# Optimization experiments

Hardware: AMD Instinct MI355X
Metric: run time of the kernel (lower is better)

## Reference

```python
import jax, jax.numpy as jnp
import numpy as np

MASK_OD = np.array([
    [False, False, False, True, True, True, True, False, False],
    [False, False, True, True, True, True, True, True, False],
    [False, True, True, True, True, True, True, True, True],
    [True, True, True, True, True, True, True, False, True],
    [True, True, True, True, True, True, True, False, True],
    [False, True, True, True, True, True, True, True, True],
    [False, False, True, True, True, True, True, True, False],
    [False, False, False, True, True, True, True, False, False]], dtype=bool)

SCALE = float(np.sqrt(128.0))  # sqrt(attn_dim)


def build_prior(num_points=52):
    # Faithful reproduction of _init_anatomical_prior (OD laterality, no flip)
    pr_grid = np.arange(196) // 14
    pc_grid = np.arange(196) % 14
    prior = np.zeros((num_points, 196), dtype=np.float32)
    vf_idx = 0
    for r in range(8):
        for c in range(9):
            if MASK_OD[r, c]:
                pr = 13 - int(r * 13 / 7)
                pc = 13 - int(c * 13 / 8)
                prior[vf_idx] = -((pr_grid - pr) ** 2 + (pc_grid - pc) ** 2) / (2.0 * 3.0 ** 2)
                vf_idx += 1
    return prior


def setup_inputs() -> dict:
    key = jax.random.key(0)
    ks = jax.random.split(key, 8)
    B, P, K, E, A = 256, 52, 196, 1024, 128
    return {
        "patches": jax.random.normal(ks[0], (B, K, E), jnp.float32),
        "queries": jax.random.normal(ks[1], (P, A), jnp.float32) * 0.02,
        "Wk": jax.random.normal(ks[2], (A, E), jnp.float32) / np.sqrt(E),
        "Wv": jax.random.normal(ks[3], (A, E), jnp.float32) / np.sqrt(E),
        "Wo": jax.random.normal(ks[4], (E, A), jnp.float32) / np.sqrt(A),
        "bo": jnp.zeros((E,), jnp.float32),
        "patch_pos": jax.random.normal(ks[5], (K, A), jnp.float32) * 0.02,
        "temperature": jnp.asarray(2.0, jnp.float32),
        "attn_prior": jnp.asarray(build_prior(P)),
    }


def reference(patches, queries, Wk, Wv, Wo, bo, patch_pos, temperature, attn_prior):
    # patches: [B, 196, E]; laterality fixed to 'OD' (no prior flip)
    keys = jnp.einsum('bke,ae->bka', patches, Wk) + patch_pos  # [B, 196, A]
    vals = jnp.einsum('bke,ae->bka', patches, Wv)              # [B, 196, A]
    logits = jnp.einsum('qa,bka->bqk', queries, keys) / SCALE  # [B, 52, 196]
    temp = jax.nn.softplus(temperature) + 0.5
    logits = (logits + attn_prior[None]) / temp
    attn_weights = jax.nn.softmax(logits, axis=-1)
    # dropout is identity in eval mode
    attended = jnp.einsum('bqk,bka->bqa', attn_weights, vals)  # [B, 52, A]
    out = jnp.einsum('bqa,ea->bqe', attended, Wo) + bo         # [B, 52, E]
    return out, attn_weights
```

## Files before the change

### kernel.cpp

```cpp
#include <hip/hip_runtime.h>

typedef __attribute__((ext_vector_type(8))) short bf16x8;
typedef __attribute__((ext_vector_type(4))) short bf16x4;
typedef __attribute__((ext_vector_type(4))) float f32x4;
typedef __attribute__((ext_vector_type(4))) float floatx4;

__device__ __forceinline__ unsigned short f2bf(float f) {
    unsigned int u = __float_as_uint(f);
    u += 0x7fffu + ((u >> 16) & 1u);
    return (unsigned short)(u >> 16);
}
__device__ __forceinline__ float bf2f_s(short h) {
    return __uint_as_float(((unsigned int)(unsigned short)h) << 16);
}

__device__ __forceinline__ bf16x8 cvt8(f32x4 lo, f32x4 hi) {
    union { unsigned int u[4]; bf16x8 v; } r;
    asm("v_cvt_pk_bf16_f32 %0, %1, %2" : "=v"(r.u[0]) : "v"(lo[0]), "v"(lo[1]));
    asm("v_cvt_pk_bf16_f32 %0, %1, %2" : "=v"(r.u[1]) : "v"(lo[2]), "v"(lo[3]));
    asm("v_cvt_pk_bf16_f32 %0, %1, %2" : "=v"(r.u[2]) : "v"(hi[0]), "v"(hi[1]));
    asm("v_cvt_pk_bf16_f32 %0, %1, %2" : "=v"(r.u[3]) : "v"(hi[2]), "v"(hi[3]));
    return r.v;
}
__device__ __forceinline__ bf16x4 cvt4(f32x4 v) {
    union { unsigned int u[2]; bf16x4 x; } r;
    asm("v_cvt_pk_bf16_f32 %0, %1, %2" : "=v"(r.u[0]) : "v"(v[0]), "v"(v[1]));
    asm("v_cvt_pk_bf16_f32 %0, %1, %2" : "=v"(r.u[1]) : "v"(v[2]), "v"(v[3]));
    return r.x;
}

__global__ void k_convert(const float* __restrict__ Wk, const float* __restrict__ Wv,
                          const float* __restrict__ Wo,
                          unsigned short* __restrict__ Wkvb, unsigned short* __restrict__ Wob) {
    int i = (blockIdx.x * blockDim.x + threadIdx.x) * 4;
    if (i < 131072) {
        floatx4 a = *reinterpret_cast<const floatx4*>(Wk + i);
        floatx4 b = *reinterpret_cast<const floatx4*>(Wv + i);
        floatx4 c = *reinterpret_cast<const floatx4*>(Wo + i);
        *reinterpret_cast<bf16x4*>(Wkvb + i)          = cvt4(a);
        *reinterpret_cast<bf16x4*>(Wkvb + 131072 + i) = cvt4(b);
        *reinterpret_cast<bf16x4*>(Wob + i)           = cvt4(c);
    }
}

__global__ __launch_bounds__(512)
void k_keysvals(const float* __restrict__ patches,
                const unsigned short* __restrict__ Wkvb,
                const float* __restrict__ patch_pos,
                unsigned short* __restrict__ kv)
{
    __shared__ unsigned short As[2][208][72];
    __shared__ unsigned short Bs[2][256][72];

    const int tid  = threadIdx.x;
    const int lane = tid & 63;
    const int w    = tid >> 6;
    const int l15  = lane & 15;
    const int lg   = lane >> 4;
    const int b    = blockIdx.x;
    const float* abase = patches + (size_t)b * 196 * 1024;

    const int brow = tid >> 1;
    const int bh   = tid & 1;
    const unsigned short* bgp = Wkvb + (size_t)brow * 1024 + bh * 32;

    f32x4  aH[7];
    bf16x8 bH[4];

    f32x4 acc[13][2];
    #pragma unroll
    for (int i = 0; i < 13; ++i) {
        acc[i][0] = (f32x4){0.f, 0.f, 0.f, 0.f};
        acc[i][1] = (f32x4){0.f, 0.f, 0.f, 0.f};
    }

    auto issue = [&](int t) {
        const int ko = t * 64;
        #pragma unroll
        for (int i = 0; i < 6; ++i) {
            int g = tid + i * 512;
            int r = g >> 4, gc = g & 15;
            aH[i] = *reinterpret_cast<const f32x4*>(abase + (size_t)r * 1024 + ko + gc * 4);
        }
        if (tid < 64) {
            int g = 3072 + tid;
            int r = g >> 4, gc = g & 15;
            aH[6] = *reinterpret_cast<const f32x4*>(abase + (size_t)r * 1024 + ko + gc * 4);
        }
        #pragma unroll
        for (int j = 0; j < 4; ++j)
            bH[j] = *reinterpret_cast<const bf16x8*>(bgp + ko + j * 8);
    };
    auto store = [&](int buf) {
        #pragma unroll
        for (int i = 0; i < 6; ++i) {
            int g = tid + i * 512;
            int r = g >> 4, gc = g & 15;
            *reinterpret_cast<bf16x4*>(&As[buf][r][gc * 4]) = cvt4(aH[i]);
        }
        if (tid < 64) {
            int g = 3072 + tid;
            int r = g >> 4, gc = g & 15;
            *reinterpret_cast<bf16x4*>(&As[buf][r][gc * 4]) = cvt4(aH[6]);
        }
        #pragma unroll
        for (int j = 0; j < 4; ++j)
            *reinterpret_cast<bf16x8*>(&Bs[buf][brow][bh * 32 + j * 8]) = bH[j];
    };
    auto compute = [&](int buf) {
        #pragma unroll
        for (int kk = 0; kk < 2; ++kk) {
            bf16x8 bf[2];
            #pragma unroll
            for (int nf = 0; nf < 2; ++nf)
                bf[nf] = *reinterpret_cast<const bf16x8*>(&Bs[buf][w * 32 + nf * 16 + l15][kk * 32 + lg * 8]);
            #pragma unroll
            for (int mf = 0; mf < 13; ++mf) {
                bf16x8 af = *reinterpret_cast<const bf16x8*>(&As[buf][mf * 16 + l15][kk * 32 + lg * 8]);
                acc[mf][0] = __builtin_amdgcn_mfma_f32_16x16x32_bf16(af, bf[0], acc[mf][0], 0, 0, 0);
                acc[mf][1] = __builtin_amdgcn_mfma_f32_16x16x32_bf16(af, bf[1], acc[mf][1], 0, 0, 0);
            }
        }
    };

    issue(0);
    store(0);
    __syncthreads();

    for (int t = 0; t < 16; ++t) {
        if (t < 15) issue(t + 1);
        compute(t & 1);
        if (t < 15) store((t + 1) & 1);
        __syncthreads();
    }

    #pragma unroll
    for (int mf = 0; mf < 13; ++mf) {
        #pragma unroll
        for (int i = 0; i < 4; ++i) {
            int ml = mf * 16 + lg * 4 + i;
            if (ml < 196) {
                #pragma unroll
                for (int nf = 0; nf < 2; ++nf) {
                    int n = w * 32 + nf * 16 + l15;
                    float v = acc[mf][nf][i];
                    if (n < 128) v += patch_pos[ml * 128 + n];
                    kv[((size_t)b * 196 + ml) * 256 + n] = f2bf(v);
                }
            }
        }
    }
}

__global__ __launch_bounds__(1024)
void k_attn(const unsigned short* __restrict__ kv,
            const float* __restrict__ queries,
            const float* __restrict__ prior,
            const float* __restrict__ temperature,
            float* __restrict__ attn_out,
            unsigned short* __restrict__ att)
{
    __shared__ unsigned short k_s[196][136];
    __shared__ unsigned short v_s[196][128];
    __shared__ unsigned short q_s[52][128];
    __shared__ float          l_s[52][196];

    const int b   = blockIdx.x;
    const int tid = threadIdx.x;
    const size_t base = (size_t)b * 196 * 256;

    for (int idx = tid; idx < 6272; idx += 1024) {
        int row = idx >> 5;
        int c   = (idx & 31) * 8;
        bf16x8 v = *reinterpret_cast<const bf16x8*>(kv + base + row * 256 + c);
        if (c < 128) *reinterpret_cast<bf16x8*>(&k_s[row][c])       = v;
        else         *reinterpret_cast<bf16x8*>(&v_s[row][c - 128]) = v;
    }
    for (int idx = tid; idx < 1664; idx += 1024) {
        int row = idx >> 5;
        int c   = (idx & 31) * 4;
        const float* qp = queries + row * 128 + c;
        bf16x4 sv;
        sv[0] = (short)f2bf(qp[0]); sv[1] = (short)f2bf(qp[1]);
        sv[2] = (short)f2bf(qp[2]); sv[3] = (short)f2bf(qp[3]);
        *reinterpret_cast<bf16x4*>(&q_s[row][c]) = sv;
    }
    __syncthreads();

    const float inv_temp  = 1.0f / (log1pf(expf(temperature[0])) + 0.5f);
    const float inv_scale = 0.08838834764831845f;

    for (int task = tid; task < 3328; task += 1024) {
        int q  = task >> 6;
        int kg = task & 63;
        if (kg < 49) {
            float dot0 = 0.f, dot1 = 0.f, dot2 = 0.f, dot3 = 0.f;
            #pragma unroll 4
            for (int c = 0; c < 128; c += 8) {
                bf16x8 qv = *reinterpret_cast<const bf16x8*>(&q_s[q][c]);
                float qf[8];
                #pragma unroll
                for (int e = 0; e < 8; ++e) qf[e] = bf2f_s(qv[e]);
                bf16x8 k0v = *reinterpret_cast<const bf16x8*>(&k_s[kg][c]);
                bf16x8 k1v = *reinterpret_cast<const bf16x8*>(&k_s[kg + 49][c]);
                bf16x8 k2v = *reinterpret_cast<const bf16x8*>(&k_s[kg + 98][c]);
                bf16x8 k3v = *reinterpret_cast<const bf16x8*>(&k_s[kg + 147][c]);
                #pragma unroll
                for (int e = 0; e < 8; ++e) {
                    dot0 += qf[e] * bf2f_s(k0v[e]);
                    dot1 += qf[e] * bf2f_s(k1v[e]);
                    dot2 += qf[e] * bf2f_s(k2v[e]);
                    dot3 += qf[e] * bf2f_s(k3v[e]);
                }
            }
            int k;
            k = kg;       l_s[q][k] = (dot0 * inv_scale + prior[q * 196 + k]) * inv_temp;
            k = kg + 49;  l_s[q][k] = (dot1 * inv_scale + prior[q * 196 + k]) * inv_temp;
            k = kg + 98;  l_s[q][k] = (dot2 * inv_scale + prior[q * 196 + k]) * inv_temp;
            k = kg + 147; l_s[q][k] = (dot3 * inv_scale + prior[q * 196 + k]) * inv_temp;
        }
    }
    __syncthreads();

    const int lane = tid & 63;
    const int wave = tid >> 6;
    for (int q = wave; q < 52; q += 16) {
        float x0 = l_s[q][lane];
        float x1 = l_s[q][lane + 64];
        float x2 = l_s[q][lane + 128];
        float x3 = (lane < 4) ? l_s[q][lane + 192] : -1e30f;
        float m = fmaxf(fmaxf(x0, x1), fmaxf(x2, x3));
        #pragma unroll
        for (int off = 32; off > 0; off >>= 1) m = fmaxf(m, __shfl_xor(m, off));
        float e0 = expf(x0 - m), e1 = expf(x1 - m), e2 = expf(x2 - m);
        float e3 = (lane < 4) ? expf(x3 - m) : 0.0f;
        float s = e0 + e1 + e2 + e3;
        #pragma unroll
        for (int off = 32; off > 0; off >>= 1) s += __shfl_xor(s, off);
        float inv = 1.0f / s;
        float* po = attn_out + ((size_t)b * 52 + q) * 196;
        float a0 = e0 * inv, a1 = e1 * inv, a2 = e2 * inv;
        l_s[q][lane]       = a0;  po[lane]       = a0;
        l_s[q][lane + 64]  = a1;  po[lane + 64]  = a1;
        l_s[q][lane + 128] = a2;  po[lane + 128] = a2;
        if (lane < 4) { float a3 = e3 * inv; l_s[q][lane + 192] = a3; po[lane + 192] = a3; }
    }
    __syncthreads();

    if (tid < 832) {
        int q  = tid >> 4;
        int a0 = (tid & 15) * 8;
        float accv[8] = {0.f, 0.f, 0.f, 0.f, 0.f, 0.f, 0.f, 0.f};
        for (int k = 0; k < 196; ++k) {
            float wgt = l_s[q][k];
            bf16x8 vv = *reinterpret_cast<const bf16x8*>(&v_s[k][a0]);
            #pragma unroll
            for (int e = 0; e < 8; ++e) accv[e] += wgt * bf2f_s(vv[e]);
        }
        bf16x8 sv;
        #pragma unroll
        for (int e = 0; e < 8; ++e) sv[e] = (short)f2bf(accv[e]);
        *reinterpret_cast<bf16x8*>(att + ((size_t)b * 52 + q) * 128 + a0) = sv;
    }
}

__global__ __launch_bounds__(512)
void k_out(const unsigned short* __restrict__ att,
           const unsigned short* __restrict__ Wob,
           const float* __restrict__ bo,
           float* __restrict__ out)
{
    __shared__ unsigned short As[64][72];
    __shared__ unsigned short Bs[256][72];

    const int tid  = threadIdx.x;
    const int lane = tid & 63;
    const int wave = tid >> 6;
    const int wm   = wave >> 2;
    const int wn   = wave & 3;
    const int l15  = lane & 15;
    const int lg   = lane >> 4;
    const int row0 = blockIdx.x * 64;
    const int e0   = blockIdx.y * 256;

    f32x4 acc[2][4];
    #pragma unroll
    for (int i = 0; i < 2; ++i)
        #pragma unroll
        for (int j = 0; j < 4; ++j)
            acc[i][j] = (f32x4){0.f, 0.f, 0.f, 0.f};

    for (int ko = 0; ko < 128; ko += 64) {
        {
            int r = tid >> 3;
            int c = (tid & 7) * 8;
            bf16x8 v = *reinterpret_cast<const bf16x8*>(att + (size_t)(row0 + r) * 128 + ko + c);
            *reinterpret_cast<bf16x8*>(&As[r][c]) = v;
        }
        {
            int r = tid >> 3;
            int c = (tid & 7) * 8;
            #pragma unroll
            for (int it = 0; it < 4; ++it) {
                bf16x8 v = *reinterpret_cast<const bf16x8*>(Wob + (size_t)(e0 + it * 64 + r) * 128 + ko + c);
                *reinterpret_cast<bf16x8*>(&Bs[it * 64 + r][c]) = v;
            }
        }
        __syncthreads();
        #pragma unroll
        for (int kk = 0; kk < 2; ++kk) {
            bf16x8 af[2], bfr[4];
            #pragma unroll
            for (int mi = 0; mi < 2; ++mi)
                af[mi] = *reinterpret_cast<const bf16x8*>(&As[wm * 32 + mi * 16 + l15][kk * 32 + lg * 8]);
            #pragma unroll
            for (int ni = 0; ni < 4; ++ni)
                bfr[ni] = *reinterpret_cast<const bf16x8*>(&Bs[wn * 64 + ni * 16 + l15][kk * 32 + lg * 8]);
            #pragma unroll
            for (int mi = 0; mi < 2; ++mi)
                #pragma unroll
                for (int ni = 0; ni < 4; ++ni)
                    acc[mi][ni] = __builtin_amdgcn_mfma_f32_16x16x32_bf16(af[mi], bfr[ni], acc[mi][ni], 0, 0, 0);
        }
        __syncthreads();
    }
    #pragma unroll
    for (int mi = 0; mi < 2; ++mi) {
        #pragma unroll
        for (int i = 0; i < 4; ++i) {
            int m = row0 + wm * 32 + mi * 16 + lg * 4 + i;
            #pragma unroll
            for (int ni = 0; ni < 4; ++ni) {
                int e = e0 + wn * 64 + ni * 16 + l15;
                out[(size_t)m * 1024 + e] = acc[mi][ni][i] + bo[e];
            }
        }
    }
}

extern "C" void kernel_launch(void* const* d_in, const int* in_sizes, int n_in,
                              void* d_out, int out_size, void* d_ws, size_t ws_size,
                              hipStream_t stream)
{
    const float* patches     = (const float*)d_in[0];
    const float* queries     = (const float*)d_in[1];
    const float* Wk          = (const float*)d_in[2];
    const float* Wv          = (const float*)d_in[3];
    const float* Wo          = (const float*)d_in[4];
    const float* bo          = (const float*)d_in[5];
    const float* patch_pos   = (const float*)d_in[6];
    const float* temperature = (const float*)d_in[7];
    const float* prior       = (const float*)d_in[8];

    float* out      = (float*)d_out;
    float* attn_out = out + (size_t)256 * 52 * 1024;

    unsigned short* Wkvb = (unsigned short*)d_ws;
    unsigned short* Wob  = Wkvb + 256 * 1024;
    unsigned short* kv   = Wob + 1024 * 128;
    unsigned short* att  = kv + (size_t)50176 * 256;

    k_convert <<<128, 256, 0, stream>>>(Wk, Wv, Wo, Wkvb, Wob);
    k_keysvals<<<256, 512, 0, stream>>>(patches, Wkvb, patch_pos, kv);
    k_attn    <<<256, 1024, 0, stream>>>(kv, queries, prior, temperature, attn_out, att);
    k_out     <<<dim3(208, 4), 512, 0, stream>>>(att, Wob, bo, out);
}
```

Before: 145.8 us.

## Fuse key/value projection with attention kernel, keep K/V in shared memory

Merges the K/V projection GEMM and the attention kernel into one 512-thread kernel per batch. K and V are written to shared memory instead of a global bf16 buffer, removing a global round trip and one launch. The GEMM main loop now uses two register prefetch sets with explicit waitcnt barriers to deepen the pipeline. In exchange the attention phase runs with half the threads per block, and the large shared memory footprint limits occupancy to one block per CU.

Result: slower. 170.7 us (+17.1%).

```diff
diff --git a/kernel.cpp b/kernel.cpp
--- a/kernel.cpp
+++ b/kernel.cpp
@@ -12,15 +12,6 @@
 }
 __device__ __forceinline__ float bf2f_s(short h) {
     return __uint_as_float(((unsigned int)(unsigned short)h) << 16);
-}
-
-__device__ __forceinline__ bf16x8 cvt8(f32x4 lo, f32x4 hi) {
-    union { unsigned int u[4]; bf16x8 v; } r;
-    asm("v_cvt_pk_bf16_f32 %0, %1, %2" : "=v"(r.u[0]) : "v"(lo[0]), "v"(lo[1]));
-    asm("v_cvt_pk_bf16_f32 %0, %1, %2" : "=v"(r.u[1]) : "v"(lo[2]), "v"(lo[3]));
-    asm("v_cvt_pk_bf16_f32 %0, %1, %2" : "=v"(r.u[2]) : "v"(hi[0]), "v"(hi[1]));
-    asm("v_cvt_pk_bf16_f32 %0, %1, %2" : "=v"(r.u[3]) : "v"(hi[2]), "v"(hi[3]));
-    return r.v;
 }
 __device__ __forceinline__ bf16x4 cvt4(f32x4 v) {
     union { unsigned int u[2]; bf16x4 x; } r;
@@ -44,13 +35,16 @@
 }
 
 __global__ __launch_bounds__(512)
-void k_keysvals(const float* __restrict__ patches,
-                const unsigned short* __restrict__ Wkvb,
-                const float* __restrict__ patch_pos,
-                unsigned short* __restrict__ kv)
+void k_fused(const float* __restrict__ patches,
+             const unsigned short* __restrict__ Wkvb,
+             const float* __restrict__ patch_pos,
+             const float* __restrict__ queries,
+             const float* __restrict__ prior,
+             const float* __restrict__ temperature,
+             float* __restrict__ attn_out,
+             unsigned short* __restrict__ att)
 {
-    __shared__ unsigned short As[2][208][72];
-    __shared__ unsigned short Bs[2][256][72];
+    __shared__ char smem[157568];
 
     const int tid  = threadIdx.x;
     const int lane = tid & 63;
@@ -64,9 +58,6 @@
     const int bh   = tid & 1;
     const unsigned short* bgp = Wkvb + (size_t)brow * 1024 + bh * 32;
 
-    f32x4  aH[7];
-    bf16x8 bH[4];
-
     f32x4 acc[13][2];
     #pragma unroll
     for (int i = 0; i < 13; ++i) {
@@ -74,65 +65,84 @@
         acc[i][1] = (f32x4){0.f, 0.f, 0.f, 0.f};
     }
 
-    auto issue = [&](int t) {
-        const int ko = t * 64;
-        #pragma unroll
-        for (int i = 0; i < 6; ++i) {
-            int g = tid + i * 512;
-            int r = g >> 4, gc = g & 15;
-            aH[i] = *reinterpret_cast<const f32x4*>(abase + (size_t)r * 1024 + ko + gc * 4);
-        }
-        if (tid < 64) {
-            int g = 3072 + tid;
-            int r = g >> 4, gc = g & 15;
-            aH[6] = *reinterpret_cast<const f32x4*>(abase + (size_t)r * 1024 + ko + gc * 4);
-        }
-        #pragma unroll
-        for (int j = 0; j < 4; ++j)
-            bH[j] = *reinterpret_cast<const bf16x8*>(bgp + ko + j * 8);
-    };
-    auto store = [&](int buf) {
-        #pragma unroll
-        for (int i = 0; i < 6; ++i) {
-            int g = tid + i * 512;
-            int r = g >> 4, gc = g & 15;
-            *reinterpret_cast<bf16x4*>(&As[buf][r][gc * 4]) = cvt4(aH[i]);
-        }
-        if (tid < 64) {
-            int g = 3072 + tid;
-            int r = g >> 4, gc = g & 15;
-            *reinterpret_cast<bf16x4*>(&As[buf][r][gc * 4]) = cvt4(aH[6]);
-        }
-        #pragma unroll
-        for (int j = 0; j < 4; ++j)
-            *reinterpret_cast<bf16x8*>(&Bs[buf][brow][bh * 32 + j * 8]) = bH[j];
-    };
-    auto compute = [&](int buf) {
-        #pragma unroll
-        for (int kk = 0; kk < 2; ++kk) {
-            bf16x8 bf[2];
-            #pragma unroll
-            for (int nf = 0; nf < 2; ++nf)
-                bf[nf] = *reinterpret_cast<const bf16x8*>(&Bs[buf][w * 32 + nf * 16 + l15][kk * 32 + lg * 8]);
-            #pragma unroll
-            for (int mf = 0; mf < 13; ++mf) {
-                bf16x8 af = *reinterpret_cast<const bf16x8*>(&As[buf][mf * 16 + l15][kk * 32 + lg * 8]);
-                acc[mf][0] = __builtin_amdgcn_mfma_f32_16x16x32_bf16(af, bf[0], acc[mf][0], 0, 0, 0);
-                acc[mf][1] = __builtin_amdgcn_mfma_f32_16x16x32_bf16(af, bf[1], acc[mf][1], 0, 0, 0);
-            }
-        }
-    };
-
-    issue(0);
-    store(0);
-    __syncthreads();
-
-    for (int t = 0; t < 16; ++t) {
-        if (t < 15) issue(t + 1);
-        compute(t & 1);
-        if (t < 15) store((t + 1) & 1);
-        __syncthreads();
-    }
+    f32x4  a0H[7], a1H[7];
+    bf16x8 b0H[4], b1H[4];
+
+#define ISSUE(AH, BH, T)                                                          \
+    do { const int ko_ = (T) * 64;                                                \
+        _Pragma("unroll")                                                         \
+        for (int i_ = 0; i_ < 6; ++i_) {                                          \
+            int g_ = tid + i_ * 512; int r_ = g_ >> 4, gc_ = g_ & 15;             \
+            AH[i_] = *reinterpret_cast<const f32x4*>(abase + (size_t)r_ * 1024 + ko_ + gc_ * 4); \
+        }                                                                         \
+        if (tid < 64) { int g_ = 3072 + tid; int r_ = g_ >> 4, gc_ = g_ & 15;     \
+            AH[6] = *reinterpret_cast<const f32x4*>(abase + (size_t)r_ * 1024 + ko_ + gc_ * 4); } \
+        _Pragma("unroll")                                                         \
+        for (int j_ = 0; j_ < 4; ++j_)                                            \
+            BH[j_] = *reinterpret_cast<const bf16x8*>(bgp + ko_ + j_ * 8);        \
+    } while (0)
+
+#define STORE(AH, BH, BUF)                                                        \
+    do { unsigned short* As_ = (unsigned short*)(smem + (BUF) * 29952);           \
+         unsigned short* Bs_ = (unsigned short*)(smem + 59904 + (BUF) * 36864);   \
+        _Pragma("unroll")                                                         \
+        for (int i_ = 0; i_ < 6; ++i_) {                                          \
+            int g_ = tid + i_ * 512; int r_ = g_ >> 4, gc_ = g_ & 15;             \
+            *reinterpret_cast<bf16x4*>(As_ + r_ * 72 + gc_ * 4) = cvt4(AH[i_]);   \
+        }                                                                         \
+        if (tid < 64) { int g_ = 3072 + tid; int r_ = g_ >> 4, gc_ = g_ & 15;     \
+            *reinterpret_cast<bf16x4*>(As_ + r_ * 72 + gc_ * 4) = cvt4(AH[6]); }  \
+        _Pragma("unroll")                                                         \
+        for (int j_ = 0; j_ < 4; ++j_)                                            \
+            *reinterpret_cast<bf16x8*>(Bs_ + brow * 72 + bh * 32 + j_ * 8) = BH[j_]; \
+    } while (0)
+
+#define COMPUTE(BUF)                                                              \
+    do { const unsigned short* As_ = (const unsigned short*)(smem + (BUF) * 29952); \
+         const unsigned short* Bs_ = (const unsigned short*)(smem + 59904 + (BUF) * 36864); \
+        _Pragma("unroll")                                                         \
+        for (int kk_ = 0; kk_ < 2; ++kk_) {                                       \
+            bf16x8 bf0 = *reinterpret_cast<const bf16x8*>(Bs_ + (w * 32 + l15) * 72 + kk_ * 32 + lg * 8);      \
+            bf16x8 bf1 = *reinterpret_cast<const bf16x8*>(Bs_ + (w * 32 + 16 + l15) * 72 + kk_ * 32 + lg * 8); \
+            _Pragma("unroll")                                                     \
+            for (int mf_ = 0; mf_ < 13; ++mf_) {                                  \
+                bf16x8 af = *reinterpret_cast<const bf16x8*>(As_ + (mf_ * 16 + l15) * 72 + kk_ * 32 + lg * 8); \
+                acc[mf_][0] = __builtin_amdgcn_mfma_f32_16x16x32_bf16(af, bf0, acc[mf_][0], 0, 0, 0); \
+                acc[mf_][1] = __builtin_amdgcn_mfma_f32_16x16x32_bf16(af, bf1, acc[mf_][1], 0, 0, 0); \
+            }                                                                     \
+        }                                                                         \
+    } while (0)
+
+#define FENCE                                                                     \
+    do { __builtin_amdgcn_sched_barrier(0);                                       \
+         asm volatile("s_waitcnt lgkmcnt(0)" ::: "memory");                       \
+         __builtin_amdgcn_s_barrier();                                            \
+         __builtin_amdgcn_sched_barrier(0); } while (0)
+
+    ISSUE(a0H, b0H, 0);
+    STORE(a0H, b0H, 0);
+    ISSUE(a1H, b1H, 1);
+    FENCE;
+
+    for (int tb = 0; tb < 16; tb += 2) {
+        if (tb + 2 < 16) ISSUE(a0H, b0H, tb + 2);
+        COMPUTE(0);
+        STORE(a1H, b1H, 1);
+        FENCE;
+        if (tb + 3 < 16) ISSUE(a1H, b1H, tb + 3);
+        COMPUTE(1);
+        if (tb + 1 < 15) STORE(a0H, b0H, 0);
+        FENCE;
+    }
+#undef ISSUE
+#undef STORE
+#undef COMPUTE
+#undef FENCE
+
+    unsigned short (*k_s)[136] = (unsigned short (*)[136])(smem);
+    unsigned short (*v_s)[128] = (unsigned short (*)[128])(smem + 53312);
+    unsigned short (*q_s)[128] = (unsigned short (*)[128])(smem + 103488);
+    float          (*l_s)[196] = (float (*)[196])(smem + 116800);
 
     #pragma unroll
     for (int mf = 0; mf < 13; ++mf) {
@@ -144,53 +154,24 @@
                 for (int nf = 0; nf < 2; ++nf) {
                     int n = w * 32 + nf * 16 + l15;
                     float v = acc[mf][nf][i];
-                    if (n < 128) v += patch_pos[ml * 128 + n];
-                    kv[((size_t)b * 196 + ml) * 256 + n] = f2bf(v);
+                    if (n < 128) k_s[ml][n] = f2bf(v + patch_pos[ml * 128 + n]);
+                    else         v_s[ml][n - 128] = f2bf(v);
                 }
             }
         }
     }
-}
-
-__global__ __launch_bounds__(1024)
-void k_attn(const unsigned short* __restrict__ kv,
-            const float* __restrict__ queries,
-            const float* __restrict__ prior,
-            const float* __restrict__ temperature,
-            float* __restrict__ attn_out,
-            unsigned short* __restrict__ att)
-{
-    __shared__ unsigned short k_s[196][136];
-    __shared__ unsigned short v_s[196][128];
-    __shared__ unsigned short q_s[52][128];
-    __shared__ float          l_s[52][196];
-
-    const int b   = blockIdx.x;
-    const int tid = threadIdx.x;
-    const size_t base = (size_t)b * 196 * 256;
-
-    for (int idx = tid; idx < 6272; idx += 1024) {
-        int row = idx >> 5;
-        int c   = (idx & 31) * 8;
-        bf16x8 v = *reinterpret_cast<const bf16x8*>(kv + base + row * 256 + c);
-        if (c < 128) *reinterpret_cast<bf16x8*>(&k_s[row][c])       = v;
-        else         *reinterpret_cast<bf16x8*>(&v_s[row][c - 128]) = v;
-    }
-    for (int idx = tid; idx < 1664; idx += 1024) {
+    for (int idx = tid; idx < 1664; idx += 512) {
         int row = idx >> 5;
         int c   = (idx & 31) * 4;
-        const float* qp = queries + row * 128 + c;
-        bf16x4 sv;
-        sv[0] = (short)f2bf(qp[0]); sv[1] = (short)f2bf(qp[1]);
-        sv[2] = (short)f2bf(qp[2]); sv[3] = (short)f2bf(qp[3]);
-        *reinterpret_cast<bf16x4*>(&q_s[row][c]) = sv;
+        f32x4 qv = *reinterpret_cast<const f32x4*>(queries + row * 128 + c);
+        *reinterpret_cast<bf16x4*>(&q_s[row][c]) = cvt4(qv);
     }
     __syncthreads();
 
     const float inv_temp  = 1.0f / (log1pf(expf(temperature[0])) + 0.5f);
     const float inv_scale = 0.08838834764831845f;
 
-    for (int task = tid; task < 3328; task += 1024) {
+    for (int task = tid; task < 3328; task += 512) {
         int q  = task >> 6;
         int kg = task & 63;
         if (kg < 49) {
@@ -222,9 +203,7 @@
     }
     __syncthreads();
 
-    const int lane = tid & 63;
-    const int wave = tid >> 6;
-    for (int q = wave; q < 52; q += 16) {
+    for (int q = w; q < 52; q += 8) {
         float x0 = l_s[q][lane];
         float x1 = l_s[q][lane + 64];
         float x2 = l_s[q][lane + 128];
@@ -247,9 +226,9 @@
     }
     __syncthreads();
 
-    if (tid < 832) {
-        int q  = tid >> 4;
-        int a0 = (tid & 15) * 8;
+    for (int task = tid; task < 832; task += 512) {
+        int q  = task >> 4;
+        int a0 = (task & 15) * 8;
         float accv[8] = {0.f, 0.f, 0.f, 0.f, 0.f, 0.f, 0.f, 0.f};
         for (int k = 0; k < 196; ++k) {
             float wgt = l_s[q][k];
@@ -356,12 +335,11 @@
     float* attn_out = out + (size_t)256 * 52 * 1024;
 
     unsigned short* Wkvb = (unsigned short*)d_ws;
-    unsigned short* Wob  = Wkvb + 256 * 1024;
-    unsigned short* kv   = Wob + 1024 * 128;
-    unsigned short* att  = kv + (size_t)50176 * 256;
-
-    k_convert <<<128, 256, 0, stream>>>(Wk, Wv, Wo, Wkvb, Wob);
-    k_keysvals<<<256, 512, 0, stream>>>(patches, Wkvb, patch_pos, kv);
-    k_attn    <<<256, 1024, 0, stream>>>(kv, queries, prior, temperature, attn_out, att);
-    k_out     <<<dim3(208, 4), 512, 0, stream>>>(att, Wob, bo, out);
-}
+    unsigned short* Wob  = Wkvb + 262144;
+    unsigned short* att  = Wob + 131072;
+
+    k_convert<<<128, 256, 0, stream>>>(Wk, Wv, Wo, Wkvb, Wob);
+    k_fused  <<<256, 512, 0, stream>>>(patches, Wkvb, patch_pos, queries, prior,
+                                       temperature, attn_out, att);
+    k_out    <<<dim3(208, 4), 512, 0, stream>>>(att, Wob, bo, out);
+}
```

## Restructure K/V projection GEMM to 1024 threads with K=32 double-buffered pipeline

Applied to the files above, without the earlier changes.

The K/V projection kernel now runs 1024 threads per block, with each wave owning a 16-column slice instead of 32. The K step per stage drops from 64 to 32, and the loop is rewritten with explicit register ping-pong buffers, sched_barrier fences and a raw s_barrier. The goal is more waves per CU to hide the latency of the fp32 patch loads and less register pressure from accumulators, at the cost of twice as many barriers and a smaller MFMA batch between syncs. The query load in the attention kernel is also vectorized.

After: 137.1 us (median of 2 runs). 1.06x faster.

```diff
diff --git a/kernel.cpp b/kernel.cpp
--- a/kernel.cpp
+++ b/kernel.cpp
@@ -12,15 +12,6 @@
 }
 __device__ __forceinline__ float bf2f_s(short h) {
     return __uint_as_float(((unsigned int)(unsigned short)h) << 16);
-}
-
-__device__ __forceinline__ bf16x8 cvt8(f32x4 lo, f32x4 hi) {
-    union { unsigned int u[4]; bf16x8 v; } r;
-    asm("v_cvt_pk_bf16_f32 %0, %1, %2" : "=v"(r.u[0]) : "v"(lo[0]), "v"(lo[1]));
-    asm("v_cvt_pk_bf16_f32 %0, %1, %2" : "=v"(r.u[1]) : "v"(lo[2]), "v"(lo[3]));
-    asm("v_cvt_pk_bf16_f32 %0, %1, %2" : "=v"(r.u[2]) : "v"(hi[0]), "v"(hi[1]));
-    asm("v_cvt_pk_bf16_f32 %0, %1, %2" : "=v"(r.u[3]) : "v"(hi[2]), "v"(hi[3]));
-    return r.v;
 }
 __device__ __forceinline__ bf16x4 cvt4(f32x4 v) {
     union { unsigned int u[2]; bf16x4 x; } r;
@@ -43,14 +34,13 @@
     }
 }
 
-__global__ __launch_bounds__(512)
+__global__ __launch_bounds__(1024, 4)
 void k_keysvals(const float* __restrict__ patches,
                 const unsigned short* __restrict__ Wkvb,
                 const float* __restrict__ patch_pos,
                 unsigned short* __restrict__ kv)
 {
-    __shared__ unsigned short As[2][208][72];
-    __shared__ unsigned short Bs[2][256][72];
+    __shared__ char smem[74240];
 
     const int tid  = threadIdx.x;
     const int lane = tid & 63;
@@ -60,79 +50,71 @@
     const int b    = blockIdx.x;
     const float* abase = patches + (size_t)b * 196 * 1024;
 
-    const int brow = tid >> 1;
-    const int bh   = tid & 1;
-    const unsigned short* bgp = Wkvb + (size_t)brow * 1024 + bh * 32;
-
-    f32x4  aH[7];
-    bf16x8 bH[4];
-
-    f32x4 acc[13][2];
+    const int ar0 = tid >> 3,          ac0 = tid & 7;
+    const int ar1 = (1024 + tid) >> 3, ac1 = (1024 + tid) & 7;
+    const int br = tid >> 2, bc = tid & 3;
+    const unsigned short* bgp = Wkvb + (size_t)br * 1024 + bc * 8;
+
+    f32x4  a0A, a0B, a1A, a1B;
+    bf16x8 b0H, b1H;
+
+    f32x4 acc[13];
     #pragma unroll
-    for (int i = 0; i < 13; ++i) {
-        acc[i][0] = (f32x4){0.f, 0.f, 0.f, 0.f};
-        acc[i][1] = (f32x4){0.f, 0.f, 0.f, 0.f};
-    }
-
-    auto issue = [&](int t) {
-        const int ko = t * 64;
-        #pragma unroll
-        for (int i = 0; i < 6; ++i) {
-            int g = tid + i * 512;
-            int r = g >> 4, gc = g & 15;
-            aH[i] = *reinterpret_cast<const f32x4*>(abase + (size_t)r * 1024 + ko + gc * 4);
-        }
-        if (tid < 64) {
-            int g = 3072 + tid;
-            int r = g >> 4, gc = g & 15;
-            aH[6] = *reinterpret_cast<const f32x4*>(abase + (size_t)r * 1024 + ko + gc * 4);
-        }
-        #pragma unroll
-        for (int j = 0; j < 4; ++j)
-            bH[j] = *reinterpret_cast<const bf16x8*>(bgp + ko + j * 8);
-    };
-    auto store = [&](int buf) {
-        #pragma unroll
-        for (int i = 0; i < 6; ++i) {
-            int g = tid + i * 512;
-            int r = g >> 4, gc = g & 15;
-            *reinterpret_cast<bf16x4*>(&As[buf][r][gc * 4]) = cvt4(aH[i]);
-        }
-        if (tid < 64) {
-            int g = 3072 + tid;
-            int r = g >> 4, gc = g & 15;
-            *reinterpret_cast<bf16x4*>(&As[buf][r][gc * 4]) = cvt4(aH[6]);
-        }
-        #pragma unroll
-        for (int j = 0; j < 4; ++j)
-            *reinterpret_cast<bf16x8*>(&Bs[buf][brow][bh * 32 + j * 8]) = bH[j];
-    };
-    auto compute = [&](int buf) {
-        #pragma unroll
-        for (int kk = 0; kk < 2; ++kk) {
-            bf16x8 bf[2];
-            #pragma unroll
-            for (int nf = 0; nf < 2; ++nf)
-                bf[nf] = *reinterpret_cast<const bf16x8*>(&Bs[buf][w * 32 + nf * 16 + l15][kk * 32 + lg * 8]);
-            #pragma unroll
-            for (int mf = 0; mf < 13; ++mf) {
-                bf16x8 af = *reinterpret_cast<const bf16x8*>(&As[buf][mf * 16 + l15][kk * 32 + lg * 8]);
-                acc[mf][0] = __builtin_amdgcn_mfma_f32_16x16x32_bf16(af, bf[0], acc[mf][0], 0, 0, 0);
-                acc[mf][1] = __builtin_amdgcn_mfma_f32_16x16x32_bf16(af, bf[1], acc[mf][1], 0, 0, 0);
-            }
-        }
-    };
-
-    issue(0);
-    store(0);
-    __syncthreads();
-
-    for (int t = 0; t < 16; ++t) {
-        if (t < 15) issue(t + 1);
-        compute(t & 1);
-        if (t < 15) store((t + 1) & 1);
-        __syncthreads();
-    }
+    for (int i = 0; i < 13; ++i) acc[i] = (f32x4){0.f, 0.f, 0.f, 0.f};
+
+#define ISSUE(AA, AB, BH, T)                                                       \
+    do { const int ko_ = (T) * 32;                                                 \
+        AA = *reinterpret_cast<const f32x4*>(abase + (size_t)ar0 * 1024 + ko_ + ac0 * 4); \
+        if (tid < 544)                                                             \
+            AB = *reinterpret_cast<const f32x4*>(abase + (size_t)ar1 * 1024 + ko_ + ac1 * 4); \
+        BH = *reinterpret_cast<const bf16x8*>(bgp + (T) * 32);                     \
+    } while (0)
+
+#define STORE(AA, AB, BH, BUF)                                                     \
+    do { unsigned short* As_ = (unsigned short*)(smem + (BUF) * 37120);            \
+         unsigned short* Bs_ = (unsigned short*)(smem + (BUF) * 37120 + 16640);    \
+        *reinterpret_cast<bf16x4*>(As_ + ar0 * 40 + ac0 * 4) = cvt4(AA);           \
+        if (tid < 544)                                                             \
+            *reinterpret_cast<bf16x4*>(As_ + ar1 * 40 + ac1 * 4) = cvt4(AB);       \
+        *reinterpret_cast<bf16x8*>(Bs_ + br * 40 + bc * 8) = BH;                   \
+    } while (0)
+
+#define COMPUTE(BUF)                                                               \
+    do { const unsigned short* As_ = (const unsigned short*)(smem + (BUF) * 37120);  \
+         const unsigned short* Bs_ = (const unsigned short*)(smem + (BUF) * 37120 + 16640); \
+        bf16x8 bf = *reinterpret_cast<const bf16x8*>(Bs_ + (w * 16 + l15) * 40 + lg * 8);  \
+        _Pragma("unroll")                                                          \
+        for (int mf_ = 0; mf_ < 13; ++mf_) {                                       \
+            bf16x8 af = *reinterpret_cast<const bf16x8*>(As_ + (mf_ * 16 + l15) * 40 + lg * 8); \
+            acc[mf_] = __builtin_amdgcn_mfma_f32_16x16x32_bf16(af, bf, acc[mf_], 0, 0, 0); \
+        }                                                                          \
+    } while (0)
+
+#define FENCE                                                                      \
+    do { __builtin_amdgcn_sched_barrier(0);                                        \
+         asm volatile("s_waitcnt lgkmcnt(0)" ::: "memory");                        \
+         __builtin_amdgcn_s_barrier();                                             \
+         __builtin_amdgcn_sched_barrier(0); } while (0)
+
+    ISSUE(a0A, a0B, b0H, 0);
+    STORE(a0A, a0B, b0H, 0);
+    ISSUE(a1A, a1B, b1H, 1);
+    FENCE;
+
+    for (int tb = 0; tb < 32; tb += 2) {
+        if (tb + 2 < 32) ISSUE(a0A, a0B, b0H, tb + 2);
+        COMPUTE(0);
+        STORE(a1A, a1B, b1H, 1);
+        FENCE;
+        if (tb + 3 < 32) ISSUE(a1A, a1B, b1H, tb + 3);
+        COMPUTE(1);
+        if (tb + 2 < 32) STORE(a0A, a0B, b0H, 0);
+        if (tb + 1 < 31) FENCE;
+    }
+#undef ISSUE
+#undef STORE
+#undef COMPUTE
+#undef FENCE
 
     #pragma unroll
     for (int mf = 0; mf < 13; ++mf) {
@@ -140,13 +122,10 @@
         for (int i = 0; i < 4; ++i) {
             int ml = mf * 16 + lg * 4 + i;
             if (ml < 196) {
-                #pragma unroll
-                for (int nf = 0; nf < 2; ++nf) {
-                    int n = w * 32 + nf * 16 + l15;
-                    float v = acc[mf][nf][i];
-                    if (n < 128) v += patch_pos[ml * 128 + n];
-                    kv[((size_t)b * 196 + ml) * 256 + n] = f2bf(v);
-                }
+                int n = w * 16 + l15;
+                float v = acc[mf][i];
+                if (n < 128) v += patch_pos[ml * 128 + n];
+                kv[((size_t)b * 196 + ml) * 256 + n] = f2bf(v);
             }
         }
     }
@@ -179,11 +158,8 @@
     for (int idx = tid; idx < 1664; idx += 1024) {
         int row = idx >> 5;
         int c   = (idx & 31) * 4;
-        const float* qp = queries + row * 128 + c;
-        bf16x4 sv;
-        sv[0] = (short)f2bf(qp[0]); sv[1] = (short)f2bf(qp[1]);
-        sv[2] = (short)f2bf(qp[2]); sv[3] = (short)f2bf(qp[3]);
-        *reinterpret_cast<bf16x4*>(&q_s[row][c]) = sv;
+        f32x4 qv = *reinterpret_cast<const f32x4*>(queries + row * 128 + c);
+        *reinterpret_cast<bf16x4*>(&q_s[row][c]) = cvt4(qv);
     }
     __syncthreads();
 
@@ -356,12 +332,12 @@
     float* attn_out = out + (size_t)256 * 52 * 1024;
 
     unsigned short* Wkvb = (unsigned short*)d_ws;
-    unsigned short* Wob  = Wkvb + 256 * 1024;
-    unsigned short* kv   = Wob + 1024 * 128;
+    unsigned short* Wob  = Wkvb + 262144;
+    unsigned short* kv   = Wob + 131072;
     unsigned short* att  = kv + (size_t)50176 * 256;
 
     k_convert <<<128, 256, 0, stream>>>(Wk, Wv, Wo, Wkvb, Wob);
-    k_keysvals<<<256, 512, 0, stream>>>(patches, Wkvb, patch_pos, kv);
+    k_keysvals<<<256, 1024, 0, stream>>>(patches, Wkvb, patch_pos, kv);
     k_attn    <<<256, 1024, 0, stream>>>(kv, queries, prior, temperature, attn_out, att);
     k_out     <<<dim3(208, 4), 512, 0, stream>>>(att, Wob, bo, out);
 }
```
